# Performance work log

Measured on AMD Instinct MI355X. Metric: run time of the kernel, lower is better.

Reference implementation:

```python
import jax, jax.numpy as jnp
import numpy as np

# Static config matching init_kwargs / input_specs
B, CIN, H, W = 4, 64, 128, 128
COUT, K, DG = 64, 3, 8
STRIDE, PAD, DIL = 1, 1, 1
HO = (H + 2 * PAD - DIL * (K - 1) - 1) // STRIDE + 1
WO = (W + 2 * PAD - DIL * (K - 1) - 1) // STRIDE + 1
KK = K * K
CG = CIN // DG  # channels per deformable group


def setup_inputs() -> dict:
    key = jax.random.key(0)
    k1, k2, k3, k4 = jax.random.split(key, 4)
    x = jax.random.normal(k1, (B, CIN, H, W), jnp.float32)
    offset = jax.random.normal(k2, (B, 2 * DG * KK, HO, WO), jnp.float32)
    s = 1.0 / np.sqrt(CIN * KK)  # matches reset_parameters stdv / fan_in bound
    weight = jax.random.uniform(k3, (COUT, CIN, K, K), jnp.float32, -s, s)
    bias = jax.random.uniform(k4, (COUT,), jnp.float32, -s, s)
    return {"x": x, "offset": offset, "weight": weight, "bias": bias}


def _deform_conv(x, offset, weight, bias):
    # offset layout (DCNv1): [B, DG * KK * 2, Ho, Wo], per kernel point (dy, dx)
    off = offset.reshape(B, DG, KK, 2, HO, WO)
    khs = (jnp.repeat(jnp.arange(K), K) * DIL).astype(jnp.float32)  # [KK] kernel dy
    kws = (jnp.tile(jnp.arange(K), K) * DIL).astype(jnp.float32)    # [KK] kernel dx
    gy = (jnp.arange(HO) * STRIDE - PAD).astype(jnp.float32)        # [Ho] base y
    gx = (jnp.arange(WO) * STRIDE - PAD).astype(jnp.float32)        # [Wo] base x
    # sampling positions: [B, DG, KK, Ho, Wo]
    py = gy[None, None, None, :, None] + khs[None, None, :, None, None] + off[:, :, :, 0]
    px = gx[None, None, None, None, :] + kws[None, None, :, None, None] + off[:, :, :, 1]
    y0 = jnp.floor(py)
    x0 = jnp.floor(px)
    ly = py - y0  # fractional parts
    lx = px - x0
    xg = x.reshape(B, DG, CG, H * W)  # channels grouped by deformable group

    def corner(yc, xc, wgt):
        # zero-padded bilinear: out-of-bounds corners contribute 0
        valid = (yc >= 0) & (yc < H) & (xc >= 0) & (xc < W)
        idx = (jnp.clip(yc, 0, H - 1) * W + jnp.clip(xc, 0, W - 1)).astype(jnp.int32)
        v = jnp.take_along_axis(xg, idx.reshape(B, DG, 1, KK * HO * WO), axis=3)
        v = v.reshape(B, DG, CG, KK, HO, WO)
        w = jnp.where(valid, wgt, 0.0)  # [B, DG, KK, Ho, Wo]
        return v * w[:, :, None]

    cols = (corner(y0, x0, (1.0 - ly) * (1.0 - lx))
            + corner(y0, x0 + 1.0, (1.0 - ly) * lx)
            + corner(y0 + 1.0, x0, ly * (1.0 - lx))
            + corner(y0 + 1.0, x0 + 1.0, ly * lx))  # [B, DG, CG, KK, Ho, Wo]

    wk = weight.reshape(COUT, DG, CG, KK)  # groups == 1
    out = jnp.einsum('bgcpyx,ogcp->boyx', cols, wk)
    return out + bias[None, :, None, None]


def reference(x, offset, weight, bias):
    return _deform_conv(x, offset, weight, bias)
```

## Files before the change

### kernel.cpp

```cpp
#include <hip/hip_runtime.h>

#define BB    4
#define CINT  64
#define HH    128
#define WW    128
#define COUT  64
#define DGN   8
#define CG    8
#define KKN   9
#define HO    128
#define WO    128
#define HOWO  16384
#define HWSZ  (HH * WW)
#define NCHUNK 18

typedef __bf16 bf16x8 __attribute__((ext_vector_type(8)));
typedef float  f32x4  __attribute__((ext_vector_type(4)));

static __device__ __forceinline__ ushort f2bf(float f) {
    unsigned u = __builtin_bit_cast(unsigned, f);
    u += 0x7fffu + ((u >> 16) & 1u);
    return (ushort)(u >> 16);
}
static __device__ __forceinline__ float bf2f(ushort u) {
    return __builtin_bit_cast(float, (unsigned)u << 16);
}

__global__ void prep_w(const float* __restrict__ wgt, uint4* __restrict__ wout) {
    int i = blockIdx.x * 256 + threadIdx.x;
    if (i >= NCHUNK * 4 * 64) return;
    int lane = i & 63;
    int mt   = (i >> 6) & 3;
    int kt   = i >> 8;
    int m = lane & 15, quad = lane >> 4;
    int o = mt * 16 + m;
    union { ushort u[8]; uint4 v; } pk;
#pragma unroll
    for (int j = 0; j < 8; ++j) {
        int k   = kt * 32 + quad * 8 + j;
        int gkk = k >> 3, c = k & 7;
        int g   = gkk / 9, kk = gkk - 9 * g;
        pk.u[j] = f2bf(wgt[(o * CINT + g * CG + c) * KKN + kk]);
    }
    wout[i] = pk.v;
}

__global__ void prep_x(const float* __restrict__ x, uint4* __restrict__ xh) {
    int i  = blockIdx.x * 256 + threadIdx.x;
    int yx = i & (HWSZ - 1);
    int bg = i >> 14;
    const float* xp = x + (size_t)bg * CG * HWSZ + yx;
    union { ushort u[8]; uint4 v; } pk;
#pragma unroll
    for (int c = 0; c < CG; ++c) pk.u[c] = f2bf(xp[c * HWSZ]);
    xh[i] = pk.v;
}

__global__ __launch_bounds__(256, 6) void dcn_mfma(
    const uint4* __restrict__ xh, const float* __restrict__ off,
    const uint4* __restrict__ wq, const float* __restrict__ bias,
    float* __restrict__ out)
{
    __shared__ __align__(16) ushort col[2][64][40];
    __shared__ float sbias[COUT];

    const int tid  = threadIdx.x;
    const int wave = tid >> 6;
    const int lane = tid & 63;
    const int px   = tid & 63;
    const int p    = wave;

    const int pix_base = blockIdx.x * 64;
    const int b        = pix_base >> 14;
    const int rem_base = pix_base & 16383;
    const int rem      = rem_base + px;
    const int ho = rem >> 7, wo = rem & 127;
    const float fy0 = (float)(ho - 1);
    const float fx0 = (float)(wo - 1);

    if (tid < COUT) sbias[tid] = bias[tid];

    f32x4 acc[4];
#pragma unroll
    for (int mt = 0; mt < 4; ++mt) acc[mt] = (f32x4){0.f, 0.f, 0.f, 0.f};

    auto produce = [&](int ch) {
        int gkk = ch * 4 + p;
        int g = gkk / 9, kk = gkk - 9 * g;
        const float* offp = off + ((size_t)((b * DGN + g) * KKN + kk) * 2) * HOWO + rem;
        float dy = offp[0];
        float dx = offp[HOWO];
        float py  = fy0 + (float)(kk / 3) + dy;
        float pxx = fx0 + (float)(kk - (kk / 3) * 3) + dx;
        float y0f = floorf(py), x0f = floorf(pxx);
        int y0 = (int)y0f, x0 = (int)x0f;
        float ly = py - y0f, lx = pxx - x0f;
        float hy = 1.f - ly, hx = 1.f - lx;
        float w00 = hy * hx, w01 = hy * lx, w10 = ly * hx, w11 = ly * lx;
        int y1 = y0 + 1, x1 = x0 + 1;
        bool vy0 = (unsigned)y0 < (unsigned)HH, vy1 = (unsigned)y1 < (unsigned)HH;
        bool vx0 = (unsigned)x0 < (unsigned)WW, vx1 = (unsigned)x1 < (unsigned)WW;
        if (!(vy0 && vx0)) w00 = 0.f;
        if (!(vy0 && vx1)) w01 = 0.f;
        if (!(vy1 && vx0)) w10 = 0.f;
        if (!(vy1 && vx1)) w11 = 0.f;
        int y0c = min(max(y0, 0), HH - 1), y1c = min(max(y1, 0), HH - 1);
        int x0c = min(max(x0, 0), WW - 1), x1c = min(max(x1, 0), WW - 1);
        const uint4* xgp = xh + (size_t)(b * DGN + g) * HWSZ;
        uint4 q00 = xgp[y0c * WW + x0c];
        uint4 q01 = xgp[y0c * WW + x1c];
        uint4 q10 = xgp[y1c * WW + x0c];
        uint4 q11 = xgp[y1c * WW + x1c];
        const ushort* u00 = (const ushort*)&q00;
        const ushort* u01 = (const ushort*)&q01;
        const ushort* u10 = (const ushort*)&q10;
        const ushort* u11 = (const ushort*)&q11;
        union { ushort u[8]; uint4 v; } pk;
#pragma unroll
        for (int c = 0; c < CG; ++c) {
            float v = w00 * bf2f(u00[c]) + w01 * bf2f(u01[c])
                    + w10 * bf2f(u10[c]) + w11 * bf2f(u11[c]);
            pk.u[c] = f2bf(v);
        }
        *(uint4*)&col[ch & 1][px][p * 8] = pk.v;
    };

    produce(0);

    const int brow  = wave * 16 + (lane & 15);
    const int bkoff = (lane >> 4) * 8;

    for (int ch = 0; ch < NCHUNK; ++ch) {
        __syncthreads();
        bf16x8 bfrag = *(const bf16x8*)&col[ch & 1][brow][bkoff];
#pragma unroll
        for (int mt = 0; mt < 4; ++mt) {
            bf16x8 afrag = __builtin_bit_cast(bf16x8, wq[(ch * 4 + mt) * 64 + lane]);
            acc[mt] = __builtin_amdgcn_mfma_f32_16x16x32_bf16(afrag, bfrag, acc[mt], 0, 0, 0);
        }
        if (ch + 1 < NCHUNK) produce(ch + 1);
    }

    const int n = lane & 15, quad = lane >> 4;
    const int rem_out = rem_base + wave * 16 + n;
    float* outp = out + (size_t)b * COUT * HOWO + rem_out;
#pragma unroll
    for (int mt = 0; mt < 4; ++mt) {
#pragma unroll
        for (int r = 0; r < 4; ++r) {
            int o = mt * 16 + quad * 4 + r;
            outp[(size_t)o * HOWO] = acc[mt][r] + sbias[o];
        }
    }
}

extern "C" void kernel_launch(void* const* d_in, const int* in_sizes, int n_in,
                              void* d_out, int out_size, void* d_ws, size_t ws_size,
                              hipStream_t stream) {
    const float* x    = (const float*)d_in[0];
    const float* off  = (const float*)d_in[1];
    const float* wgt  = (const float*)d_in[2];
    const float* bias = (const float*)d_in[3];
    float* out = (float*)d_out;

    uint4* xh = (uint4*)d_ws;
    uint4* wq = (uint4*)((char*)d_ws + 8388608);

    prep_x<<<dim3(BB * DGN * HWSZ / 256), dim3(256), 0, stream>>>(x, xh);
    prep_w<<<dim3(NCHUNK), dim3(256), 0, stream>>>(wgt, wq);
    dcn_mfma<<<dim3(BB * HO * WO / 64), dim3(256), 0, stream>>>(xh, off, wq, bias, out);
}
```

Measured before the change: 125.0 us.

## Compute bilinear fragments in registers with padded input and prefetched gathers

Pads the bf16 input by two pixels on each side so bilinear corner loads need no bounds checks or masking. Each lane now builds its MFMA B-fragment directly in registers, removing the shared-memory column buffer and per-chunk block barriers. Offsets and corner gathers for the next chunk are issued one step ahead to overlap memory latency with MFMA work. The two prep kernels are merged into one launch. The cost is more registers per thread and a lower occupancy hint.

```diff
diff --git a/kernel.cpp b/kernel.cpp
--- a/kernel.cpp
+++ b/kernel.cpp
@@ -4,15 +4,18 @@
 #define CINT  64
 #define HH    128
 #define WW    128
-#define COUT  64
+#define COUTN 64
 #define DGN   8
-#define CG    8
+#define CGN   8
 #define KKN   9
-#define HO    128
-#define WO    128
 #define HOWO  16384
 #define HWSZ  (HH * WW)
+#define HP    132
+#define WP    132
+#define HWP   (HP * WP)
+#define NXG   (BB * DGN * HWP)
 #define NCHUNK 18
+#define NWBLK  18
 
 typedef __bf16 bf16x8 __attribute__((ext_vector_type(8)));
 typedef float  f32x4  __attribute__((ext_vector_type(4)));
@@ -22,134 +25,145 @@
     u += 0x7fffu + ((u >> 16) & 1u);
     return (ushort)(u >> 16);
 }
-static __device__ __forceinline__ float bf2f(ushort u) {
-    return __builtin_bit_cast(float, (unsigned)u << 16);
+
+__global__ __launch_bounds__(256) void prep(
+    const float* __restrict__ x, const float* __restrict__ wgt,
+    uint4* __restrict__ xh, uint4* __restrict__ wq)
+{
+    const int bid = blockIdx.x;
+    const int tid = threadIdx.x;
+    if (bid < NWBLK) {
+        int i = bid * 256 + tid;
+        int lane = i & 63;
+        int mt   = (i >> 6) & 3;
+        int kt   = i >> 8;
+        int m = lane & 15, quad = lane >> 4;
+        int o = mt * 16 + m;
+        union { ushort u[8]; uint4 v; } pk;
+#pragma unroll
+        for (int j = 0; j < 8; ++j) {
+            int k   = kt * 32 + quad * 8 + j;
+            int gkk = k >> 3, c = k & 7;
+            int g   = gkk / 9, kk = gkk - 9 * g;
+            pk.u[j] = f2bf(wgt[(o * CINT + g * CGN + c) * KKN + kk]);
+        }
+        wq[i] = pk.v;
+        return;
+    }
+    int j = (bid - NWBLK) * 256 + tid;
+    if (j >= NXG) return;
+    int bg = j / HWP;
+    int r  = j - bg * HWP;
+    int yp = r / WP;
+    int xp = r - yp * WP;
+    union { ushort u[8]; uint4 v; } pk;
+    pk.v.x = pk.v.y = pk.v.z = pk.v.w = 0u;
+    if (yp >= 2 && yp <= 129 && xp >= 2 && xp <= 129) {
+        const float* src = x + (size_t)bg * CGN * HWSZ + (yp - 2) * WW + (xp - 2);
+#pragma unroll
+        for (int c = 0; c < CGN; ++c) pk.u[c] = f2bf(src[c * HWSZ]);
+    }
+    xh[j] = pk.v;
 }
 
-__global__ void prep_w(const float* __restrict__ wgt, uint4* __restrict__ wout) {
-    int i = blockIdx.x * 256 + threadIdx.x;
-    if (i >= NCHUNK * 4 * 64) return;
-    int lane = i & 63;
-    int mt   = (i >> 6) & 3;
-    int kt   = i >> 8;
-    int m = lane & 15, quad = lane >> 4;
-    int o = mt * 16 + m;
-    union { ushort u[8]; uint4 v; } pk;
-#pragma unroll
-    for (int j = 0; j < 8; ++j) {
-        int k   = kt * 32 + quad * 8 + j;
-        int gkk = k >> 3, c = k & 7;
-        int g   = gkk / 9, kk = gkk - 9 * g;
-        pk.u[j] = f2bf(wgt[(o * CINT + g * CG + c) * KKN + kk]);
-    }
-    wout[i] = pk.v;
-}
-
-__global__ void prep_x(const float* __restrict__ x, uint4* __restrict__ xh) {
-    int i  = blockIdx.x * 256 + threadIdx.x;
-    int yx = i & (HWSZ - 1);
-    int bg = i >> 14;
-    const float* xp = x + (size_t)bg * CG * HWSZ + yx;
-    union { ushort u[8]; uint4 v; } pk;
-#pragma unroll
-    for (int c = 0; c < CG; ++c) pk.u[c] = f2bf(xp[c * HWSZ]);
-    xh[i] = pk.v;
-}
-
-__global__ __launch_bounds__(256, 6) void dcn_mfma(
+__global__ __launch_bounds__(256, 4) void dcn_mfma(
     const uint4* __restrict__ xh, const float* __restrict__ off,
     const uint4* __restrict__ wq, const float* __restrict__ bias,
     float* __restrict__ out)
 {
-    __shared__ __align__(16) ushort col[2][64][40];
-    __shared__ float sbias[COUT];
-
     const int tid  = threadIdx.x;
     const int wave = tid >> 6;
     const int lane = tid & 63;
-    const int px   = tid & 63;
-    const int p    = wave;
+    const int q    = lane >> 4;
+    const int n    = lane & 15;
 
-    const int pix_base = blockIdx.x * 64;
-    const int b        = pix_base >> 14;
-    const int rem_base = pix_base & 16383;
-    const int rem      = rem_base + px;
+    const int wid     = blockIdx.x * 4 + wave;
+    const int pixbase = wid * 16;
+    const int b       = pixbase >> 14;
+    const int rem     = (pixbase & 16383) + n;
     const int ho = rem >> 7, wo = rem & 127;
     const float fy0 = (float)(ho - 1);
     const float fx0 = (float)(wo - 1);
 
-    if (tid < COUT) sbias[tid] = bias[tid];
+    const float* offp = off + (size_t)(b * 72 + q) * 2 * HOWO + rem;
+
+    float lofy[4], lofx[4];
+#pragma unroll
+    for (int c0 = 0; c0 < 4; ++c0) {
+        lofy[c0] = offp[(size_t)c0 * 8 * HOWO];
+        lofx[c0] = offp[(size_t)c0 * 8 * HOWO + HOWO];
+    }
 
     f32x4 acc[4];
 #pragma unroll
     for (int mt = 0; mt < 4; ++mt) acc[mt] = (f32x4){0.f, 0.f, 0.f, 0.f};
 
-    auto produce = [&](int ch) {
-        int gkk = ch * 4 + p;
-        int g = gkk / 9, kk = gkk - 9 * g;
-        const float* offp = off + ((size_t)((b * DGN + g) * KKN + kk) * 2) * HOWO + rem;
-        float dy = offp[0];
-        float dx = offp[HOWO];
-        float py  = fy0 + (float)(kk / 3) + dy;
-        float pxx = fx0 + (float)(kk - (kk / 3) * 3) + dx;
+    const int xbase = b * DGN * HWP;
+
+    int g = 0, kk = q;
+    uint4 c00, c01, c10, c11, n00, n01, n10, n11;
+    float w00, w01, w10, w11, v00, v01, v10, v11;
+
+    auto issue = [&](int ch, uint4& r00, uint4& r01, uint4& r10, uint4& r11,
+                     float& u00, float& u01, float& u10, float& u11) {
+        int kh = (kk * 11) >> 5;
+        int kw = kk - 3 * kh;
+        float py  = fy0 + (float)kh + lofy[ch & 3];
+        float pxx = fx0 + (float)kw + lofx[ch & 3];
         float y0f = floorf(py), x0f = floorf(pxx);
-        int y0 = (int)y0f, x0 = (int)x0f;
         float ly = py - y0f, lx = pxx - x0f;
         float hy = 1.f - ly, hx = 1.f - lx;
-        float w00 = hy * hx, w01 = hy * lx, w10 = ly * hx, w11 = ly * lx;
-        int y1 = y0 + 1, x1 = x0 + 1;
-        bool vy0 = (unsigned)y0 < (unsigned)HH, vy1 = (unsigned)y1 < (unsigned)HH;
-        bool vx0 = (unsigned)x0 < (unsigned)WW, vx1 = (unsigned)x1 < (unsigned)WW;
-        if (!(vy0 && vx0)) w00 = 0.f;
-        if (!(vy0 && vx1)) w01 = 0.f;
-        if (!(vy1 && vx0)) w10 = 0.f;
-        if (!(vy1 && vx1)) w11 = 0.f;
-        int y0c = min(max(y0, 0), HH - 1), y1c = min(max(y1, 0), HH - 1);
-        int x0c = min(max(x0, 0), WW - 1), x1c = min(max(x1, 0), WW - 1);
-        const uint4* xgp = xh + (size_t)(b * DGN + g) * HWSZ;
-        uint4 q00 = xgp[y0c * WW + x0c];
-        uint4 q01 = xgp[y0c * WW + x1c];
-        uint4 q10 = xgp[y1c * WW + x0c];
-        uint4 q11 = xgp[y1c * WW + x1c];
-        const ushort* u00 = (const ushort*)&q00;
-        const ushort* u01 = (const ushort*)&q01;
-        const ushort* u10 = (const ushort*)&q10;
-        const ushort* u11 = (const ushort*)&q11;
-        union { ushort u[8]; uint4 v; } pk;
-#pragma unroll
-        for (int c = 0; c < CG; ++c) {
-            float v = w00 * bf2f(u00[c]) + w01 * bf2f(u01[c])
-                    + w10 * bf2f(u10[c]) + w11 * bf2f(u11[c]);
-            pk.u[c] = f2bf(v);
-        }
-        *(uint4*)&col[ch & 1][px][p * 8] = pk.v;
+        u00 = hy * hx; u01 = hy * lx; u10 = ly * hx; u11 = ly * lx;
+        int y0 = (int)y0f, x0 = (int)x0f;
+        y0 = min(max(y0, -2), HH);
+        x0 = min(max(x0, -2), WW);
+        const uint4* p = xh + (xbase + g * HWP + (y0 + 2) * WP + (x0 + 2));
+        r00 = p[0]; r01 = p[1]; r10 = p[WP]; r11 = p[WP + 1];
+        kk += 4; if (kk >= KKN) { kk -= KKN; ++g; }
     };
 
-    produce(0);
+    issue(0, c00, c01, c10, c11, w00, w01, w10, w11);
 
-    const int brow  = wave * 16 + (lane & 15);
-    const int bkoff = (lane >> 4) * 8;
+#pragma unroll
+    for (int ch = 0; ch < NCHUNK; ++ch) {
+        if (ch + 4 < NCHUNK) {
+            lofy[(ch + 4) & 3] = offp[(size_t)(ch + 4) * 8 * HOWO];
+            lofx[(ch + 4) & 3] = offp[(size_t)(ch + 4) * 8 * HOWO + HOWO];
+        }
+        if (ch + 1 < NCHUNK)
+            issue(ch + 1, n00, n01, n10, n11, v00, v01, v10, v11);
 
-    for (int ch = 0; ch < NCHUNK; ++ch) {
-        __syncthreads();
-        bf16x8 bfrag = *(const bf16x8*)&col[ch & 1][brow][bkoff];
+        const __bf16* a00 = (const __bf16*)&c00;
+        const __bf16* a01 = (const __bf16*)&c01;
+        const __bf16* a10 = (const __bf16*)&c10;
+        const __bf16* a11 = (const __bf16*)&c11;
+        bf16x8 bfrag;
+#pragma unroll
+        for (int cc = 0; cc < 8; ++cc) {
+            float v = w00 * (float)a00[cc] + w01 * (float)a01[cc]
+                    + w10 * (float)a10[cc] + w11 * (float)a11[cc];
+            bfrag[cc] = (__bf16)v;
+        }
 #pragma unroll
         for (int mt = 0; mt < 4; ++mt) {
             bf16x8 afrag = __builtin_bit_cast(bf16x8, wq[(ch * 4 + mt) * 64 + lane]);
             acc[mt] = __builtin_amdgcn_mfma_f32_16x16x32_bf16(afrag, bfrag, acc[mt], 0, 0, 0);
         }
-        if (ch + 1 < NCHUNK) produce(ch + 1);
+        if (ch + 1 < NCHUNK) {
+            c00 = n00; c01 = n01; c10 = n10; c11 = n11;
+            w00 = v00; w01 = v01; w10 = v10; w11 = v11;
+        }
     }
 
-    const int n = lane & 15, quad = lane >> 4;
-    const int rem_out = rem_base + wave * 16 + n;
-    float* outp = out + (size_t)b * COUT * HOWO + rem_out;
+    const int rem_out = (pixbase & 16383) + n;
+    float* outp = out + (size_t)b * COUTN * HOWO + rem_out;
 #pragma unroll
     for (int mt = 0; mt < 4; ++mt) {
+        f32x4 bv = *(const f32x4*)(bias + mt * 16 + q * 4);
 #pragma unroll
         for (int r = 0; r < 4; ++r) {
-            int o = mt * 16 + quad * 4 + r;
-            outp[(size_t)o * HOWO] = acc[mt][r] + sbias[o];
+            int o = mt * 16 + q * 4 + r;
+            outp[(size_t)o * HOWO] = acc[mt][r] + bv[r];
         }
     }
 }
@@ -164,9 +178,9 @@
     float* out = (float*)d_out;
 
     uint4* xh = (uint4*)d_ws;
-    uint4* wq = (uint4*)((char*)d_ws + 8388608);
+    uint4* wq = (uint4*)((char*)d_ws + (size_t)NXG * 16);
 
-    prep_x<<<dim3(BB * DGN * HWSZ / 256), dim3(256), 0, stream>>>(x, xh);
-    prep_w<<<dim3(NCHUNK), dim3(256), 0, stream>>>(wgt, wq);
-    dcn_mfma<<<dim3(BB * HO * WO / 64), dim3(256), 0, stream>>>(xh, off, wq, bias, out);
+    const int xblocks = (NXG + 255) / 256;
+    prep<<<dim3(NWBLK + xblocks), dim3(256), 0, stream>>>(x, wgt, xh, wq);
+    dcn_mfma<<<dim3(BB * HOWO / 64), dim3(256), 0, stream>>>(xh, off, wq, bias, out);
 }
```

Measured after the change: 123.3 us. About the same (-1.3%).
